# Performance work log

Measured on AMD Instinct MI355X. Metric: run time of the kernel, lower is better.

The kernel has to match this reference:

```python
import jax, jax.numpy as jnp
import numpy as np

IN_DIM = 256
HID = 384
HEADS = 6
NH1 = HID // HEADS  # 64 per-head hidden in layer1
N = 3072
SLOPE_GAT = 0.2   # LeakyReLU inside GAT attention
SLOPE_ACT = 0.01  # default nn.LeakyReLU / F.leaky_relu slope


def _leaky(x, s):
    return jnp.where(x >= 0, x, s * x)


def _gat_sublayer(h, mask, W, a, heads, nh, concat):
    # h: [N, F_in], mask: [N, N] bool, W: [heads*nh, F_in], a: [2*nh]
    n = h.shape[0]
    g = (h @ W.T).reshape(n, heads, nh)  # [N, H, F]
    # e[i,j,h] = leakyrelu(<g_i, a_l> + <g_j, a_r>)  (avoids O(N^2) concat)
    sl = jnp.einsum('nhf,f->nh', g, a[:nh])
    sr = jnp.einsum('nhf,f->nh', g, a[nh:])
    e = _leaky(sl[:, None, :] + sr[None, :, :], SLOPE_GAT)  # [N, N, H]
    e = jnp.where(mask[:, :, None], e, jnp.float32(-10000.0))
    att = jax.nn.softmax(e, axis=1)  # softmax over source nodes j
    out = jnp.einsum('ijh,jhf->ihf', att, g)
    return out.reshape(n, heads * nh) if concat else out.mean(axis=1)


def _gat(x, mask, W1, a1, W2, a2):
    x = _gat_sublayer(x, mask, W1, a1, HEADS, NH1, True)   # [N, HID]
    x = jax.nn.elu(x)
    return _gat_sublayer(x, mask, W2, a2, 1, IN_DIM, False)  # [N, IN_DIM]


def setup_inputs() -> dict:
    key = jax.random.key(0)
    ks = iter(jax.random.split(key, 32))
    d = {
        'feature': jax.random.normal(next(ks), (1, N, IN_DIM), jnp.float32),
        'adj': jax.random.randint(next(ks), (1, N, N), 0, 2, jnp.int32),
        'doc_num': 16,
        'sect_num': 192,
    }
    def w(shape, scale=0.05):
        return jax.random.normal(next(ks), shape, jnp.float32) * scale
    for br in ('sent', 'sect', 'doc'):
        d[f'W1_{br}'] = w((HID, IN_DIM))
        d[f'a1_{br}'] = w((2 * NH1,))
        d[f'W2_{br}'] = w((IN_DIM, HID))
        d[f'a2_{br}'] = w((2 * IN_DIM,))
    d['fusion_W'] = w((IN_DIM, 3 * IN_DIM)); d['fusion_b'] = jnp.zeros((IN_DIM,), jnp.float32)
    d['ffn_W0'] = w((HID, IN_DIM)); d['ffn_b0'] = jnp.zeros((HID,), jnp.float32)
    d['ffn_W1'] = w((HID, HID)); d['ffn_b1'] = jnp.zeros((HID,), jnp.float32)
    d['ffn_W2'] = w((IN_DIM, HID)); d['ffn_b2'] = jnp.zeros((IN_DIM,), jnp.float32)
    return d


def reference(feature, adj, doc_num, sect_num,
              W1_sent, a1_sent, W2_sent, a2_sent,
              W1_sect, a1_sect, W2_sect, a2_sect,
              W1_doc, a1_doc, W2_doc, a2_doc,
              fusion_W, fusion_b,
              ffn_W0, ffn_b0, ffn_W1, ffn_b1, ffn_W2, ffn_b2):
    f = feature[0]          # [N, D]
    n = f.shape[0]
    A = adj[0] != 0         # [N, N]
    cols = jnp.arange(n)
    sent_mask = A & (cols < n - sect_num - doc_num)[None, :]
    sect_mask = A & (cols >= n - sect_num - doc_num)[None, :] & (cols < n - doc_num)[None, :]
    doc_mask = A & (cols >= n - doc_num)[None, :]

    f_sent = _gat(f, sent_mask, W1_sent, a1_sent, W2_sent, a2_sent) + f
    f_sect = _gat(f, sect_mask, W1_sect, a1_sect, W2_sect, a2_sect) + f
    f_doc = _gat(f, doc_mask, W1_doc, a1_doc, W2_doc, a2_doc) + f

    fused = jnp.concatenate([f_doc, f_sect, f_sent], axis=-1)  # [N, 3D]
    fused = _leaky(fused @ fusion_W.T + fusion_b, SLOPE_ACT)
    h = _leaky(fused @ ffn_W0.T + ffn_b0, SLOPE_ACT)
    h = _leaky(h @ ffn_W1.T + ffn_b1, SLOPE_ACT)
    h = _leaky(h @ ffn_W2.T + ffn_b2, SLOPE_ACT)
    return (h + f)[None]    # [1, N, D]
```

## Files before the change

kernel.cpp:

```cpp
#include <hip/hip_runtime.h>
#include <stdint.h>

#define N_NODES 3072
#define D_IN    256
#define HIDDEN  384
#define HEADS   6
#define NH1     64
#define C1      1152
#define C2      768
#define MASK_ULL   48
#define MASK_BYTES 384
#define MASK_BSTRIDE ((size_t)N_NODES * MASK_BYTES)
#define QS      4
#define LOG2E   1.4426950408889634f

typedef __bf16 bf16;
typedef __bf16 bf16x8 __attribute__((ext_vector_type(8)));
typedef __bf16 bf16x4 __attribute__((ext_vector_type(4)));
typedef float  f32x4  __attribute__((ext_vector_type(4)));

__device__ __forceinline__ void atomAddF(float* p, float v) {
  __hip_atomic_fetch_add(p, v, __ATOMIC_RELAXED, __HIP_MEMORY_SCOPE_AGENT);
}
__device__ __forceinline__ float fexp2(float x) {
  float r; asm("v_exp_f32 %0, %1" : "=v"(r) : "v"(x)); return r;
}
__device__ __forceinline__ int bnd32(int jlo, int jhi, int len, int q, int Qb) {
  return (q >= Qb) ? ((jhi + 31) & ~31) : ((jlo + (len * q) / Qb) & ~31);
}

struct CastArgs {
  const float* src[11];
  bf16*        dst[11];
  int          cum4[12];
};

__global__ __launch_bounds__(256) void cast_all_kernel(CastArgs A) {
  int g = blockIdx.x * 256 + threadIdx.x;
  int j = 0;
#pragma unroll
  for (int k = 1; k < 11; ++k) j += (g >= A.cum4[k]);
  int e = (g - A.cum4[j]) * 4;
  float4 v = *(const float4*)(A.src[j] + e);
  bf16x4 o = { (bf16)v.x, (bf16)v.y, (bf16)v.z, (bf16)v.w };
  *(bf16x4*)(A.dst[j] + e) = o;
}

__global__ __launch_bounds__(256) void pack_adj_kernel(const int* __restrict__ adj,
                                                       unsigned long long* __restrict__ maskU,
                                                       const int* __restrict__ dnum,
                                                       const int* __restrict__ snum) {
  int dn = dnum[0], sn = snum[0];
  int bb1 = N_NODES - sn - dn, bb2 = N_NODES - dn;
  int row = blockIdx.x;
  const int* ar = adj + (size_t)row * N_NODES;
  int lane = threadIdx.x & 63, wave = threadIdx.x >> 6;
#pragma unroll
  for (int it = 0; it < N_NODES / 256; ++it) {
    int j = it * 256 + wave * 64 + lane;
    bool a = ar[j] != 0;
    unsigned long long m0 = __ballot(a && (j < bb1));
    unsigned long long m1 = __ballot(a && (j >= bb1) && (j < bb2));
    unsigned long long m2 = __ballot(a && (j >= bb2));
    if (lane == 0) {
      size_t o = (size_t)row * MASK_ULL + it * 4 + wave;
      maskU[o] = m0;
      maskU[o + (size_t)N_NODES * MASK_ULL] = m1;
      maskU[o + 2 * (size_t)N_NODES * MASK_ULL] = m2;
    }
  }
}

template<int C>
__global__ __launch_bounds__(256) void pack_kernel(const bf16* __restrict__ src,
                                                   bf16* __restrict__ dst) {
  __shared__ bf16 t[64][72];
  int j0 = blockIdx.x * 64, f0 = blockIdx.y * 64;
  int rr = threadIdx.x >> 4;
  int cc = (threadIdx.x & 15) * 4;
#pragma unroll
  for (int p = 0; p < 4; ++p) {
    int r = p * 16 + rr;
    *(bf16x4*)&t[r][cc] = *(const bf16x4*)&src[(size_t)(j0 + r) * C + f0 + cc];
  }
  __syncthreads();
  int f = threadIdx.x & 63, g = threadIdx.x >> 6;
#pragma unroll
  for (int q = 0; q < 2; ++q) {
    int p = g * 2 + q;
    bf16x8 v = { t[p*8+0][f], t[p*8+1][f], t[p*8+2][f], t[p*8+3][f],
                 t[p*8+4][f], t[p*8+5][f], t[p*8+6][f], t[p*8+7][f] };
    *(bf16x8*)&dst[ ((size_t)((j0 >> 3) + p) * C + f0 + f) * 8 ] = v;
  }
}

template<int NCPB, int NH>
__global__ __launch_bounds__(256) void head_proj_kernel(
    const bf16* __restrict__ g, int ldg,
    const float* __restrict__ a0, const float* __restrict__ a1, const float* __restrict__ a2,
    float* __restrict__ elp, float* __restrict__ eln,
    float* __restrict__ erp, float* __restrict__ ern) {
  int c = blockIdx.y;
  int i = blockIdx.x * 16 + (threadIdx.x >> 4);
  int b = c / NCPB;
  const float* a = (b == 0) ? a0 : (b == 1) ? a1 : a2;
  int f0 = (threadIdx.x & 15) * (NH / 16);
  const bf16* gr = g + (size_t)i * ldg + c * NH + f0;
  float accl = 0.f, accr = 0.f;
#pragma unroll
  for (int k = 0; k < NH / 16; k += 4) {
    bf16x4 v = *(const bf16x4*)&gr[k];
#pragma unroll
    for (int e = 0; e < 4; ++e) {
      float gv = (float)v[e];
      accl += gv * a[f0 + k + e];
      accr += gv * a[NH + f0 + k + e];
    }
  }
#pragma unroll
  for (int m = 1; m < 16; m <<= 1) {
    accl += __shfl_xor(accl, m, 64);
    accr += __shfl_xor(accr, m, 64);
  }
  if ((threadIdx.x & 15) == 0) {
    int o = c * N_NODES + i;
    elp[o] = fexp2(accl * LOG2E);
    eln[o] = fexp2(0.2f * accl * LOG2E);
    erp[o] = fexp2(accr * LOG2E);
    ern[o] = fexp2(0.2f * accr * LOG2E);
  }
}

__global__ __launch_bounds__(256) void colmean_kernel(const bf16* __restrict__ g, int C,
                                                      float* __restrict__ out) {
  int c = blockIdx.x * 256 + threadIdx.x;
  if (c >= C) return;
  int r0 = blockIdx.y * 128;
  float s = 0.f;
  for (int r = r0; r < r0 + 128; ++r) s += (float)g[(size_t)r * C + c];
  atomAddF(&out[c], s * (1.0f / N_NODES));
}

template<bool BIAS, bool LEAKY, bool RES, bool F32OUT>
__global__ __launch_bounds__(256) void gemm64_kernel(
    const bf16* __restrict__ A, int lda, int aZoff,
    const bf16* __restrict__ B0, const bf16* __restrict__ B1, const bf16* __restrict__ B2,
    int ldb, void* __restrict__ Cout, int ldc, int cZoff, int K,
    const float* __restrict__ bias, const float* __restrict__ res) {
  __shared__ bf16 As[64 * 64];
  __shared__ bf16 Bs[64 * 64];
  int z = blockIdx.z;
  const bf16* Ab = A + (size_t)z * aZoff;
  const bf16* Bb = (z == 0) ? B0 : (z == 1) ? B1 : B2;
  int m0 = blockIdx.x * 64, n0 = blockIdx.y * 64;
  int tid = threadIdx.x;
  int lane = tid & 63, wave = tid >> 6;
  int wm = wave >> 1, wn = wave & 1;
  int l15 = lane & 15, lk = lane >> 4;
  f32x4 acc[2][2] = {};
  for (int kt = 0; kt < K; kt += 64) {
#pragma unroll
    for (int h = 0; h < 2; ++h) {
      int u = h * 256 + tid;
      int r = u >> 3, up = u & 7;
      int ul = up ^ (r & 7);
      *(bf16x8*)&As[r * 64 + up * 8] = *(const bf16x8*)&Ab[(size_t)(m0 + r) * lda + kt + ul * 8];
      *(bf16x8*)&Bs[r * 64 + up * 8] = *(const bf16x8*)&Bb[(size_t)(n0 + r) * ldb + kt + ul * 8];
    }
    __syncthreads();
#pragma unroll
    for (int s = 0; s < 2; ++s) {
      bf16x8 af[2], bfr[2];
      int u = s * 4 + lk;
#pragma unroll
      for (int mi = 0; mi < 2; ++mi) {
        int r = wm * 32 + mi * 16 + l15;
        af[mi] = *(const bf16x8*)&As[r * 64 + (u ^ (r & 7)) * 8];
      }
#pragma unroll
      for (int ni = 0; ni < 2; ++ni) {
        int r = wn * 32 + ni * 16 + l15;
        bfr[ni] = *(const bf16x8*)&Bs[r * 64 + (u ^ (r & 7)) * 8];
      }
#pragma unroll
      for (int mi = 0; mi < 2; ++mi)
#pragma unroll
        for (int ni = 0; ni < 2; ++ni)
          acc[mi][ni] = __builtin_amdgcn_mfma_f32_16x16x32_bf16(af[mi], bfr[ni], acc[mi][ni], 0, 0, 0);
    }
    __syncthreads();
  }
#pragma unroll
  for (int mi = 0; mi < 2; ++mi)
#pragma unroll
    for (int ni = 0; ni < 2; ++ni)
#pragma unroll
      for (int r = 0; r < 4; ++r) {
        int i = m0 + wm * 32 + mi * 16 + lk * 4 + r;
        int col = z * cZoff + n0 + wn * 32 + ni * 16 + l15;
        float v = acc[mi][ni][r];
        if (BIAS) v += bias[col];
        if (LEAKY) v = (v >= 0.f) ? v : 0.01f * v;
        if (RES) v += res[(size_t)i * ldc + col];
        if (F32OUT) ((float*)Cout)[(size_t)i * ldc + col] = v;
        else        ((bf16*)Cout)[(size_t)i * ldc + col] = (bf16)v;
      }
}

template<bool L1>
__global__ __launch_bounds__(256) void att_kernel(
    const bf16* __restrict__ gP,
    const float* __restrict__ elpA, const float* __restrict__ elnA,
    const float* __restrict__ erpA, const float* __restrict__ ernA,
    const unsigned char* __restrict__ maskB,
    const int* __restrict__ dnum, const int* __restrict__ snum,
    float* __restrict__ accP, float* __restrict__ lP) {
  constexpr int C = L1 ? C1 : C2;
  constexpr int NSENT = L1 ? 6 : 4;
  int c = blockIdx.y;
  int b = L1 ? (c / 6) : (c >> 2);
  int colbase = L1 ? c * 64 : (b * 256 + (c & 3) * 64);
  int sidx = L1 ? c : b;
  int q = blockIdx.z;
  int Qb = (b == 0) ? QS : 1;
  if (q >= Qb) return;
  int dn = dnum[0], sn = snum[0];
  int bb1 = N_NODES - sn - dn, bb2 = N_NODES - dn;
  int jlo = (b == 0) ? 0 : (b == 1) ? bb1 : bb2;
  int jhi = (b == 0) ? bb1 : (b == 1) ? bb2 : N_NODES;
  int len = jhi - jlo;
  int wlo = bnd32(jlo, jhi, len, q, Qb);
  int whi = bnd32(jlo, jhi, len, q + 1, Qb);
  if (wlo >= whi) return;

  int wave = threadIdx.x >> 6, lane = threadIdx.x & 63;
  int l15 = lane & 15, lk = lane >> 4;
  int row0 = blockIdx.x * 64 + wave * 16;
  int ip = row0 + l15;
  float elp = elpA[sidx * N_NODES + ip];
  float eln = elnA[sidx * N_NODES + ip];
  const float* erpB = erpA + sidx * N_NODES;
  const float* ernB = ernA + sidx * N_NODES;
  const unsigned char* mrow = maskB + (size_t)b * MASK_BSTRIDE + (size_t)ip * MASK_BYTES;
  bf16x8 ones;
#pragma unroll
  for (int e = 0; e < 8; ++e) ones[e] = (bf16)1.0f;
  f32x4 acc[4] = {};
  f32x4 accl = {};
  for (int jt = wlo; jt < whi; jt += 32) {
    int jb = jt + lk * 8;
    unsigned int mb = mrow[jb >> 3];
    float4 p0 = *(const float4*)&erpB[jb];
    float4 p1 = *(const float4*)&erpB[jb + 4];
    float4 n0 = *(const float4*)&ernB[jb];
    float4 n1 = *(const float4*)&ernB[jb + 4];
    float pv[8] = { p0.x, p0.y, p0.z, p0.w, p1.x, p1.y, p1.z, p1.w };
    float nv[8] = { n0.x, n0.y, n0.z, n0.w, n1.x, n1.y, n1.z, n1.w };
    bf16x8 a8;
#pragma unroll
    for (int e = 0; e < 8; ++e) {
      float z = elp * pv[e];
      float w = eln * nv[e];
      float p = (z >= 1.f) ? z : w;
      p = ((mb >> e) & 1u) ? p : 0.f;
      a8[e] = (bf16)p;
    }
    size_t pbase = (size_t)(jb >> 3) * C * 8;
#pragma unroll
    for (int nf = 0; nf < 4; ++nf) {
      bf16x8 b8 = *(const bf16x8*)&gP[pbase + (size_t)(colbase + nf * 16 + l15) * 8];
      acc[nf] = __builtin_amdgcn_mfma_f32_16x16x32_bf16(a8, b8, acc[nf], 0, 0, 0);
    }
    accl = __builtin_amdgcn_mfma_f32_16x16x32_bf16(a8, ones, accl, 0, 0, 0);
  }
  int slot = (b == 0) ? (c * QS + q) : (NSENT * QS + (c - NSENT));
  float* ap = accP + ((size_t)slot * N_NODES + row0) * 64;
#pragma unroll
  for (int nf = 0; nf < 4; ++nf)
#pragma unroll
    for (int r = 0; r < 4; ++r)
      ap[(lk * 4 + r) * 64 + nf * 16 + l15] = acc[nf][r];
  if (l15 == 0) {
#pragma unroll
    for (int r = 0; r < 4; ++r)
      lP[(size_t)slot * N_NODES + row0 + lk * 4 + r] = accl[r];
  }
}

__global__ __launch_bounds__(256) void fin1_kernel(
    const float* __restrict__ accP, const float* __restrict__ lP,
    const float* __restrict__ gm, const int* __restrict__ dnum, const int* __restrict__ snum,
    bf16* __restrict__ out1) {
  int t = blockIdx.x * 256 + threadIdx.x;
  int i = t / (C1 / 8), f0 = (t - i * (C1 / 8)) * 8;
  int c = f0 >> 6;
  int b = c / 6;
  int dn = dnum[0], sn = snum[0];
  int bb1 = N_NODES - sn - dn, bb2 = N_NODES - dn;
  int jlo = (b == 0) ? 0 : (b == 1) ? bb1 : bb2;
  int jhi = (b == 0) ? bb1 : (b == 1) ? bb2 : N_NODES;
  int len = jhi - jlo;
  int Qb = (b == 0) ? QS : 1;
  float l = 0.f;
  float a[8] = {0.f,0.f,0.f,0.f,0.f,0.f,0.f,0.f};
  if (len > 0) {
    for (int q = 0; q < Qb; ++q) {
      if (bnd32(jlo, jhi, len, q, Qb) >= bnd32(jlo, jhi, len, q + 1, Qb)) continue;
      int slot = (b == 0) ? (c * QS + q) : (6 * QS + (c - 6));
      l += lP[(size_t)slot * N_NODES + i];
      const float* ap = &accP[((size_t)slot * N_NODES + i) * 64 + (f0 & 63)];
      f32x4 v0 = *(const f32x4*)ap, v1 = *(const f32x4*)(ap + 4);
#pragma unroll
      for (int e = 0; e < 4; ++e) { a[e] += v0[e]; a[e + 4] += v1[e]; }
    }
  }
  float inv = (l > 0.f) ? 1.f / l : 0.f;
  bf16x8 o;
#pragma unroll
  for (int e = 0; e < 8; ++e) {
    float v = (l > 0.f) ? a[e] * inv : gm[f0 + e];
    v = (v > 0.f) ? v : (__expf(v) - 1.f);
    o[e] = (bf16)v;
  }
  *(bf16x8*)&out1[(size_t)i * C1 + f0] = o;
}

__global__ __launch_bounds__(256) void fin2_kernel(
    const float* __restrict__ accP, const float* __restrict__ lP,
    const float* __restrict__ gm, const float* __restrict__ feat,
    const int* __restrict__ dnum, const int* __restrict__ snum,
    bf16* __restrict__ fused) {
  int t = blockIdx.x * 256 + threadIdx.x;
  int i = t / (C2 / 8), f0 = (t - i * (C2 / 8)) * 8;
  int b = f0 >> 8;
  int fi = f0 & 255;
  int fc = (f0 >> 6) & 3;
  int c = b * 4 + fc;
  int dn = dnum[0], sn = snum[0];
  int bb1 = N_NODES - sn - dn, bb2 = N_NODES - dn;
  int jlo = (b == 0) ? 0 : (b == 1) ? bb1 : bb2;
  int jhi = (b == 0) ? bb1 : (b == 1) ? bb2 : N_NODES;
  int len = jhi - jlo;
  int Qb = (b == 0) ? QS : 1;
  float l = 0.f;
  float a[8] = {0.f,0.f,0.f,0.f,0.f,0.f,0.f,0.f};
  if (len > 0) {
    for (int q = 0; q < Qb; ++q) {
      if (bnd32(jlo, jhi, len, q, Qb) >= bnd32(jlo, jhi, len, q + 1, Qb)) continue;
      int slot = (b == 0) ? (c * QS + q) : (4 * QS + (c - 4));
      l += lP[(size_t)slot * N_NODES + i];
      const float* ap = &accP[((size_t)slot * N_NODES + i) * 64 + (f0 & 63)];
      f32x4 v0 = *(const f32x4*)ap, v1 = *(const f32x4*)(ap + 4);
#pragma unroll
      for (int e = 0; e < 4; ++e) { a[e] += v0[e]; a[e + 4] += v1[e]; }
    }
  }
  float inv = (l > 0.f) ? 1.f / l : 0.f;
  bf16x8 o;
#pragma unroll
  for (int e = 0; e < 8; ++e) {
    float v = (l > 0.f) ? a[e] * inv : gm[f0 + e];
    v += feat[(size_t)i * D_IN + fi + e];
    o[e] = (bf16)v;
  }
  *(bf16x8*)&fused[(size_t)i * C2 + (2 - b) * D_IN + fi] = o;
}

extern "C" void kernel_launch(void* const* d_in, const int* in_sizes, int n_in,
                              void* d_out, int out_size, void* d_ws, size_t ws_size,
                              hipStream_t stream) {
  (void)in_sizes; (void)n_in; (void)out_size; (void)ws_size;
  const float* feature = (const float*)d_in[0];
  const int*   adj     = (const int*)d_in[1];
  const int*   dnum    = (const int*)d_in[2];
  const int*   snum    = (const int*)d_in[3];
  const float* W1s = (const float*)d_in[4];  const float* a1s = (const float*)d_in[5];
  const float* W2s = (const float*)d_in[6];  const float* a2s = (const float*)d_in[7];
  const float* W1e = (const float*)d_in[8];  const float* a1e = (const float*)d_in[9];
  const float* W2e = (const float*)d_in[10]; const float* a2e = (const float*)d_in[11];
  const float* W1d = (const float*)d_in[12]; const float* a1d = (const float*)d_in[13];
  const float* W2d = (const float*)d_in[14]; const float* a2d = (const float*)d_in[15];
  const float* fW  = (const float*)d_in[16]; const float* fB  = (const float*)d_in[17];
  const float* w0  = (const float*)d_in[18]; const float* b0  = (const float*)d_in[19];
  const float* w1  = (const float*)d_in[20]; const float* b1  = (const float*)d_in[21];
  const float* w2  = (const float*)d_in[22]; const float* b2  = (const float*)d_in[23];

  char* ws = (char*)d_ws;
  size_t off = 0;
  auto alloc = [&](size_t bytes) { void* p = ws + off; off += (bytes + 255) & ~(size_t)255; return p; };

  unsigned long long* maskU = (unsigned long long*)alloc(3 * (size_t)N_NODES * MASK_ULL * 8);
  bf16* fbf   = (bf16*)alloc((size_t)N_NODES * D_IN * 2);
  bf16* w1b0  = (bf16*)alloc(HIDDEN * D_IN * 2);
  bf16* w1b1  = (bf16*)alloc(HIDDEN * D_IN * 2);
  bf16* w1b2  = (bf16*)alloc(HIDDEN * D_IN * 2);
  bf16* w2b0  = (bf16*)alloc(D_IN * HIDDEN * 2);
  bf16* w2b1  = (bf16*)alloc(D_IN * HIDDEN * 2);
  bf16* w2b2  = (bf16*)alloc(D_IN * HIDDEN * 2);
  bf16* wfusb = (bf16*)alloc(D_IN * C2 * 2);
  bf16* wf0b  = (bf16*)alloc(HIDDEN * D_IN * 2);
  bf16* wf1b  = (bf16*)alloc(HIDDEN * HIDDEN * 2);
  bf16* wf2b  = (bf16*)alloc(D_IN * HIDDEN * 2);
  bf16* g1    = (bf16*)alloc((size_t)N_NODES * C1 * 2);
  bf16* gP1   = (bf16*)alloc((size_t)N_NODES * C1 * 2);
  bf16* out1  = (bf16*)alloc((size_t)N_NODES * C1 * 2);
  bf16* g2    = (bf16*)alloc((size_t)N_NODES * C2 * 2);
  bf16* gP2   = (bf16*)alloc((size_t)N_NODES * C2 * 2);
  bf16* fusedB= (bf16*)alloc((size_t)N_NODES * C2 * 2);
  bf16* h0    = (bf16*)alloc((size_t)N_NODES * D_IN * 2);
  bf16* h1    = (bf16*)alloc((size_t)N_NODES * HIDDEN * 2);
  bf16* h2    = (bf16*)alloc((size_t)N_NODES * HIDDEN * 2);
  float* elp1 = (float*)alloc(18 * N_NODES * 4);
  float* eln1 = (float*)alloc(18 * N_NODES * 4);
  float* erp1 = (float*)alloc(18 * N_NODES * 4);
  float* ern1 = (float*)alloc(18 * N_NODES * 4);
  float* elp2 = (float*)alloc(3 * N_NODES * 4);
  float* eln2 = (float*)alloc(3 * N_NODES * 4);
  float* erp2 = (float*)alloc(3 * N_NODES * 4);
  float* ern2 = (float*)alloc(3 * N_NODES * 4);
  float* accU = (float*)alloc((size_t)36 * N_NODES * 64 * 4);
  float* lU   = (float*)alloc((size_t)36 * N_NODES * 4);
  size_t zoff = off;
  float* gm1  = (float*)alloc(C1 * 4);
  float* gm2  = (float*)alloc(C2 * 4);
  size_t zbytes = off - zoff;
  const unsigned char* maskBytes = (const unsigned char*)maskU;

  hipMemsetAsync(ws + zoff, 0, zbytes, stream);

  CastArgs ca;
  {
    const float* srcs[11] = { feature, W1s, W1e, W1d, W2s, W2e, W2d, fW, w0, w1, w2 };
    bf16* dsts[11] = { fbf, w1b0, w1b1, w1b2, w2b0, w2b1, w2b2, wfusb, wf0b, wf1b, wf2b };
    int counts[11] = { N_NODES*D_IN, HIDDEN*D_IN, HIDDEN*D_IN, HIDDEN*D_IN,
                       D_IN*HIDDEN, D_IN*HIDDEN, D_IN*HIDDEN, D_IN*C2,
                       HIDDEN*D_IN, HIDDEN*HIDDEN, D_IN*HIDDEN };
    int cum = 0;
    for (int k = 0; k < 11; ++k) { ca.src[k] = srcs[k]; ca.dst[k] = dsts[k]; ca.cum4[k] = cum; cum += counts[k] / 4; }
    ca.cum4[11] = cum;
    cast_all_kernel<<<cum / 256, 256, 0, stream>>>(ca);
  }
  pack_adj_kernel<<<N_NODES, 256, 0, stream>>>(adj, maskU, dnum, snum);
  gemm64_kernel<false,false,false,false><<<dim3(48,6,3), 256, 0, stream>>>(
      fbf, D_IN, 0, w1b0, w1b1, w1b2, D_IN, g1, C1, HIDDEN, D_IN, nullptr, nullptr);
  pack_kernel<C1><<<dim3(48,18), 256, 0, stream>>>(g1, gP1);
  head_proj_kernel<HEADS, NH1><<<dim3(192,18), 256, 0, stream>>>(g1, C1, a1s, a1e, a1d, elp1, eln1, erp1, ern1);
  colmean_kernel<<<dim3((C1 + 255) / 256, 24), 256, 0, stream>>>(g1, C1, gm1);
  att_kernel<true><<<dim3(48, 18, QS), 256, 0, stream>>>(gP1, elp1, eln1, erp1, ern1, maskBytes, dnum, snum, accU, lU);
  fin1_kernel<<<N_NODES * (C1 / 8) / 256, 256, 0, stream>>>(accU, lU, gm1, dnum, snum, out1);
  gemm64_kernel<false,false,false,false><<<dim3(48,4,3), 256, 0, stream>>>(
      out1, C1, HIDDEN, w2b0, w2b1, w2b2, HIDDEN, g2, C2, D_IN, HIDDEN, nullptr, nullptr);
  pack_kernel<C2><<<dim3(48,12), 256, 0, stream>>>(g2, gP2);
  head_proj_kernel<1, D_IN><<<dim3(192,3), 256, 0, stream>>>(g2, C2, a2s, a2e, a2d, elp2, eln2, erp2, ern2);
  colmean_kernel<<<dim3((C2 + 255) / 256, 24), 256, 0, stream>>>(g2, C2, gm2);
  att_kernel<false><<<dim3(48, 12, QS), 256, 0, stream>>>(gP2, elp2, eln2, erp2, ern2, maskBytes, dnum, snum, accU, lU);
  fin2_kernel<<<N_NODES * (C2 / 8) / 256, 256, 0, stream>>>(accU, lU, gm2, feature, dnum, snum, fusedB);
  gemm64_kernel<true,true,false,false><<<dim3(48,4,1), 256, 0, stream>>>(
      fusedB, C2, 0, wfusb, wfusb, wfusb, C2, h0, D_IN, 0, C2, fB, nullptr);
  gemm64_kernel<true,true,false,false><<<dim3(48,6,1), 256, 0, stream>>>(
      h0, D_IN, 0, wf0b, wf0b, wf0b, D_IN, h1, HIDDEN, 0, D_IN, b0, nullptr);
  gemm64_kernel<true,true,false,false><<<dim3(48,6,1), 256, 0, stream>>>(
      h1, HIDDEN, 0, wf1b, wf1b, wf1b, HIDDEN, h2, HIDDEN, 0, HIDDEN, b1, nullptr);
  gemm64_kernel<true,true,true,true><<<dim3(48,4,1), 256, 0, stream>>>(
      h2, HIDDEN, 0, wf2b, wf2b, wf2b, HIDDEN, d_out, D_IN, 0, HIDDEN, b2, feature);
}
```

Before: 321.0 us.

## Register-tile attention over four row groups, prefetch stream, fuse column mean into pack

The attention kernel now has each wave process 64 rows as four 16-row groups. Each loaded block of projected features and source-side exponentials is therefore reused four times. The next 32-column tile is prefetched into registers while the current one is computed. The grid shrinks in x and the sentence-branch split count grows from 4 to 6 so the machine stays occupied, and the workspace slots are resized to match. The separate column-mean kernel is removed and its sums are accumulated in the pack kernel through atomics. The cost is much higher register pressure from 16 accumulator tiles plus the prefetch buffers, which may lower occupancy.

New measurement: 285.5 us. -11.1%, faster.

```diff
diff --git a/kernel.cpp b/kernel.cpp
--- a/kernel.cpp
+++ b/kernel.cpp
@@ -11,7 +11,7 @@
 #define MASK_ULL   48
 #define MASK_BYTES 384
 #define MASK_BSTRIDE ((size_t)N_NODES * MASK_BYTES)
-#define QS      4
+#define QS      6
 #define LOG2E   1.4426950408889634f
 
 typedef __bf16 bf16;
@@ -73,7 +73,8 @@
 
 template<int C>
 __global__ __launch_bounds__(256) void pack_kernel(const bf16* __restrict__ src,
-                                                   bf16* __restrict__ dst) {
+                                                   bf16* __restrict__ dst,
+                                                   float* __restrict__ gm) {
   __shared__ bf16 t[64][72];
   int j0 = blockIdx.x * 64, f0 = blockIdx.y * 64;
   int rr = threadIdx.x >> 4;
@@ -92,6 +93,10 @@
                  t[p*8+4][f], t[p*8+5][f], t[p*8+6][f], t[p*8+7][f] };
     *(bf16x8*)&dst[ ((size_t)((j0 >> 3) + p) * C + f0 + f) * 8 ] = v;
   }
+  float s = 0.f;
+#pragma unroll
+  for (int k = 0; k < 16; ++k) s += (float)t[g * 16 + k][f];
+  atomAddF(&gm[f0 + f], s * (1.0f / N_NODES));
 }
 
 template<int NCPB, int NH>
@@ -129,16 +134,6 @@
     erp[o] = fexp2(accr * LOG2E);
     ern[o] = fexp2(0.2f * accr * LOG2E);
   }
-}
-
-__global__ __launch_bounds__(256) void colmean_kernel(const bf16* __restrict__ g, int C,
-                                                      float* __restrict__ out) {
-  int c = blockIdx.x * 256 + threadIdx.x;
-  if (c >= C) return;
-  int r0 = blockIdx.y * 128;
-  float s = 0.f;
-  for (int r = r0; r < r0 + 128; ++r) s += (float)g[(size_t)r * C + c];
-  atomAddF(&out[c], s * (1.0f / N_NODES));
 }
 
 template<bool BIAS, bool LEAKY, bool RES, bool F32OUT>
@@ -207,6 +202,32 @@
       }
 }
 
+struct Stream {
+  float4 p0, p1, n0, n1;
+  unsigned int m0, m1, m2, m3;
+  bf16x8 b0, b1, b2, b3;
+};
+
+template<int C>
+__device__ __forceinline__ void load_stream(
+    Stream& s, int jb,
+    const float* __restrict__ erpB, const float* __restrict__ ernB,
+    const unsigned char* mr0, const unsigned char* mr1,
+    const unsigned char* mr2, const unsigned char* mr3,
+    const bf16* __restrict__ gPl) {
+  s.p0 = *(const float4*)&erpB[jb];
+  s.p1 = *(const float4*)&erpB[jb + 4];
+  s.n0 = *(const float4*)&ernB[jb];
+  s.n1 = *(const float4*)&ernB[jb + 4];
+  int mo = jb >> 3;
+  s.m0 = mr0[mo]; s.m1 = mr1[mo]; s.m2 = mr2[mo]; s.m3 = mr3[mo];
+  const bf16* gp = gPl + (size_t)mo * C * 8;
+  s.b0 = *(const bf16x8*)(gp + 0);
+  s.b1 = *(const bf16x8*)(gp + 128);
+  s.b2 = *(const bf16x8*)(gp + 256);
+  s.b3 = *(const bf16x8*)(gp + 384);
+}
+
 template<bool L1>
 __global__ __launch_bounds__(256) void att_kernel(
     const bf16* __restrict__ gP,
@@ -216,7 +237,6 @@
     const int* __restrict__ dnum, const int* __restrict__ snum,
     float* __restrict__ accP, float* __restrict__ lP) {
   constexpr int C = L1 ? C1 : C2;
-  constexpr int NSENT = L1 ? 6 : 4;
   int c = blockIdx.y;
   int b = L1 ? (c / 6) : (c >> 2);
   int colbase = L1 ? c * 64 : (b * 256 + (c & 3) * 64);
@@ -235,55 +255,76 @@
 
   int wave = threadIdx.x >> 6, lane = threadIdx.x & 63;
   int l15 = lane & 15, lk = lane >> 4;
-  int row0 = blockIdx.x * 64 + wave * 16;
-  int ip = row0 + l15;
-  float elp = elpA[sidx * N_NODES + ip];
-  float eln = elnA[sidx * N_NODES + ip];
+  int row0 = blockIdx.x * 256 + wave * 64;
+  float elp[4], eln[4];
+  const unsigned char* mr0;
+  const unsigned char* mr1;
+  const unsigned char* mr2;
+  const unsigned char* mr3;
+  {
+    const unsigned char* mbase = maskB + (size_t)b * MASK_BSTRIDE;
+#pragma unroll
+    for (int rg = 0; rg < 4; ++rg) {
+      int ip = row0 + rg * 16 + l15;
+      elp[rg] = elpA[sidx * N_NODES + ip];
+      eln[rg] = elnA[sidx * N_NODES + ip];
+    }
+    mr0 = mbase + (size_t)(row0 + 0 * 16 + l15) * MASK_BYTES;
+    mr1 = mbase + (size_t)(row0 + 1 * 16 + l15) * MASK_BYTES;
+    mr2 = mbase + (size_t)(row0 + 2 * 16 + l15) * MASK_BYTES;
+    mr3 = mbase + (size_t)(row0 + 3 * 16 + l15) * MASK_BYTES;
+  }
   const float* erpB = erpA + sidx * N_NODES;
   const float* ernB = ernA + sidx * N_NODES;
-  const unsigned char* mrow = maskB + (size_t)b * MASK_BSTRIDE + (size_t)ip * MASK_BYTES;
+  const bf16* gPl = gP + (size_t)(colbase + l15) * 8;
   bf16x8 ones;
 #pragma unroll
   for (int e = 0; e < 8; ++e) ones[e] = (bf16)1.0f;
-  f32x4 acc[4] = {};
-  f32x4 accl = {};
+  f32x4 acc[4][4] = {};
+  f32x4 accl[4] = {};
+
+  Stream s;
+  load_stream<C>(s, wlo + lk * 8, erpB, ernB, mr0, mr1, mr2, mr3, gPl);
   for (int jt = wlo; jt < whi; jt += 32) {
-    int jb = jt + lk * 8;
-    unsigned int mb = mrow[jb >> 3];
-    float4 p0 = *(const float4*)&erpB[jb];
-    float4 p1 = *(const float4*)&erpB[jb + 4];
-    float4 n0 = *(const float4*)&ernB[jb];
-    float4 n1 = *(const float4*)&ernB[jb + 4];
-    float pv[8] = { p0.x, p0.y, p0.z, p0.w, p1.x, p1.y, p1.z, p1.w };
-    float nv[8] = { n0.x, n0.y, n0.z, n0.w, n1.x, n1.y, n1.z, n1.w };
-    bf16x8 a8;
-#pragma unroll
-    for (int e = 0; e < 8; ++e) {
-      float z = elp * pv[e];
-      float w = eln * nv[e];
-      float p = (z >= 1.f) ? z : w;
-      p = ((mb >> e) & 1u) ? p : 0.f;
-      a8[e] = (bf16)p;
-    }
-    size_t pbase = (size_t)(jb >> 3) * C * 8;
-#pragma unroll
-    for (int nf = 0; nf < 4; ++nf) {
-      bf16x8 b8 = *(const bf16x8*)&gP[pbase + (size_t)(colbase + nf * 16 + l15) * 8];
-      acc[nf] = __builtin_amdgcn_mfma_f32_16x16x32_bf16(a8, b8, acc[nf], 0, 0, 0);
-    }
-    accl = __builtin_amdgcn_mfma_f32_16x16x32_bf16(a8, ones, accl, 0, 0, 0);
-  }
-  int slot = (b == 0) ? (c * QS + q) : (NSENT * QS + (c - NSENT));
+    Stream cur = s;
+    int nxt = jt + 32;
+    if (nxt < whi) load_stream<C>(s, nxt + lk * 8, erpB, ernB, mr0, mr1, mr2, mr3, gPl);
+    float pv[8] = { cur.p0.x, cur.p0.y, cur.p0.z, cur.p0.w, cur.p1.x, cur.p1.y, cur.p1.z, cur.p1.w };
+    float nv[8] = { cur.n0.x, cur.n0.y, cur.n0.z, cur.n0.w, cur.n1.x, cur.n1.y, cur.n1.z, cur.n1.w };
+#pragma unroll
+    for (int rg = 0; rg < 4; ++rg) {
+      unsigned int mb = (rg == 0) ? cur.m0 : (rg == 1) ? cur.m1 : (rg == 2) ? cur.m2 : cur.m3;
+      bf16x8 a8;
+#pragma unroll
+      for (int e = 0; e < 8; ++e) {
+        float z = elp[rg] * pv[e];
+        float w = eln[rg] * nv[e];
+        float p = (z >= 1.f) ? z : w;
+        p = ((mb >> e) & 1u) ? p : 0.f;
+        a8[e] = (bf16)p;
+      }
+      acc[rg][0] = __builtin_amdgcn_mfma_f32_16x16x32_bf16(a8, cur.b0, acc[rg][0], 0, 0, 0);
+      acc[rg][1] = __builtin_amdgcn_mfma_f32_16x16x32_bf16(a8, cur.b1, acc[rg][1], 0, 0, 0);
+      acc[rg][2] = __builtin_amdgcn_mfma_f32_16x16x32_bf16(a8, cur.b2, acc[rg][2], 0, 0, 0);
+      acc[rg][3] = __builtin_amdgcn_mfma_f32_16x16x32_bf16(a8, cur.b3, acc[rg][3], 0, 0, 0);
+      accl[rg] = __builtin_amdgcn_mfma_f32_16x16x32_bf16(a8, ones, accl[rg], 0, 0, 0);
+    }
+  }
+  int slot = (b == 0) ? (c * QS + q) : (L1 ? (36 + (c - 6)) : (24 + (c - 4)));
   float* ap = accP + ((size_t)slot * N_NODES + row0) * 64;
 #pragma unroll
-  for (int nf = 0; nf < 4; ++nf)
-#pragma unroll
-    for (int r = 0; r < 4; ++r)
-      ap[(lk * 4 + r) * 64 + nf * 16 + l15] = acc[nf][r];
+  for (int rg = 0; rg < 4; ++rg)
+#pragma unroll
+    for (int nf = 0; nf < 4; ++nf)
+#pragma unroll
+      for (int r = 0; r < 4; ++r)
+        ap[(rg * 16 + lk * 4 + r) * 64 + nf * 16 + l15] = acc[rg][nf][r];
   if (l15 == 0) {
 #pragma unroll
-    for (int r = 0; r < 4; ++r)
-      lP[(size_t)slot * N_NODES + row0 + lk * 4 + r] = accl[r];
+    for (int rg = 0; rg < 4; ++rg)
+#pragma unroll
+      for (int r = 0; r < 4; ++r)
+        lP[(size_t)slot * N_NODES + row0 + rg * 16 + lk * 4 + r] = accl[rg][r];
   }
 }
 
@@ -306,7 +347,7 @@
   if (len > 0) {
     for (int q = 0; q < Qb; ++q) {
       if (bnd32(jlo, jhi, len, q, Qb) >= bnd32(jlo, jhi, len, q + 1, Qb)) continue;
-      int slot = (b == 0) ? (c * QS + q) : (6 * QS + (c - 6));
+      int slot = (b == 0) ? (c * QS + q) : (36 + (c - 6));
       l += lP[(size_t)slot * N_NODES + i];
       const float* ap = &accP[((size_t)slot * N_NODES + i) * 64 + (f0 & 63)];
       f32x4 v0 = *(const f32x4*)ap, v1 = *(const f32x4*)(ap + 4);
@@ -347,7 +388,7 @@
   if (len > 0) {
     for (int q = 0; q < Qb; ++q) {
       if (bnd32(jlo, jhi, len, q, Qb) >= bnd32(jlo, jhi, len, q + 1, Qb)) continue;
-      int slot = (b == 0) ? (c * QS + q) : (4 * QS + (c - 4));
+      int slot = (b == 0) ? (c * QS + q) : (24 + (c - 4));
       l += lP[(size_t)slot * N_NODES + i];
       const float* ap = &accP[((size_t)slot * N_NODES + i) * 64 + (f0 & 63)];
       f32x4 v0 = *(const f32x4*)ap, v1 = *(const f32x4*)(ap + 4);
@@ -418,8 +459,8 @@
   float* eln2 = (float*)alloc(3 * N_NODES * 4);
   float* erp2 = (float*)alloc(3 * N_NODES * 4);
   float* ern2 = (float*)alloc(3 * N_NODES * 4);
-  float* accU = (float*)alloc((size_t)36 * N_NODES * 64 * 4);
-  float* lU   = (float*)alloc((size_t)36 * N_NODES * 4);
+  float* accU = (float*)alloc((size_t)48 * N_NODES * 64 * 4);
+  float* lU   = (float*)alloc((size_t)48 * N_NODES * 4);
   size_t zoff = off;
   float* gm1  = (float*)alloc(C1 * 4);
   float* gm2  = (float*)alloc(C2 * 4);
@@ -443,17 +484,15 @@
   pack_adj_kernel<<<N_NODES, 256, 0, stream>>>(adj, maskU, dnum, snum);
   gemm64_kernel<false,false,false,false><<<dim3(48,6,3), 256, 0, stream>>>(
       fbf, D_IN, 0, w1b0, w1b1, w1b2, D_IN, g1, C1, HIDDEN, D_IN, nullptr, nullptr);
-  pack_kernel<C1><<<dim3(48,18), 256, 0, stream>>>(g1, gP1);
+  pack_kernel<C1><<<dim3(48,18), 256, 0, stream>>>(g1, gP1, gm1);
   head_proj_kernel<HEADS, NH1><<<dim3(192,18), 256, 0, stream>>>(g1, C1, a1s, a1e, a1d, elp1, eln1, erp1, ern1);
-  colmean_kernel<<<dim3((C1 + 255) / 256, 24), 256, 0, stream>>>(g1, C1, gm1);
-  att_kernel<true><<<dim3(48, 18, QS), 256, 0, stream>>>(gP1, elp1, eln1, erp1, ern1, maskBytes, dnum, snum, accU, lU);
+  att_kernel<true><<<dim3(12, 18, QS), 256, 0, stream>>>(gP1, elp1, eln1, erp1, ern1, maskBytes, dnum, snum, accU, lU);
   fin1_kernel<<<N_NODES * (C1 / 8) / 256, 256, 0, stream>>>(accU, lU, gm1, dnum, snum, out1);
   gemm64_kernel<false,false,false,false><<<dim3(48,4,3), 256, 0, stream>>>(
       out1, C1, HIDDEN, w2b0, w2b1, w2b2, HIDDEN, g2, C2, D_IN, HIDDEN, nullptr, nullptr);
-  pack_kernel<C2><<<dim3(48,12), 256, 0, stream>>>(g2, gP2);
+  pack_kernel<C2><<<dim3(48,12), 256, 0, stream>>>(g2, gP2, gm2);
   head_proj_kernel<1, D_IN><<<dim3(192,3), 256, 0, stream>>>(g2, C2, a2s, a2e, a2d, elp2, eln2, erp2, ern2);
-  colmean_kernel<<<dim3((C2 + 255) / 256, 24), 256, 0, stream>>>(g2, C2, gm2);
-  att_kernel<false><<<dim3(48, 12, QS), 256, 0, stream>>>(gP2, elp2, eln2, erp2, ern2, maskBytes, dnum, snum, accU, lU);
+  att_kernel<false><<<dim3(12, 12, QS), 256, 0, stream>>>(gP2, elp2, eln2, erp2, ern2, maskBytes, dnum, snum, accU, lU);
   fin2_kernel<<<N_NODES * (C2 / 8) / 256, 256, 0, stream>>>(accU, lU, gm2, feature, dnum, snum, fusedB);
   gemm64_kernel<true,true,false,false><<<dim3(48,4,1), 256, 0, stream>>>(
       fusedB, C2, 0, wfusb, wfusb, wfusb, C2, h0, D_IN, 0, C2, fB, nullptr);
```
